# Kernel tuning notes

Measured on AMD Instinct MI355X. Metric: run time of the kernel, lower is better.

Reference implementation:

```python
import jax, jax.numpy as jnp
import numpy as np

B, S, SEG, D = 2, 128, 128, 768
RL, H, DK = 16, 8, 64
DV = D // H            # 96, dim_value = dim // heads
NRPF = D // H          # num_rel_pos_features
N = S * RL             # 2048 attention tokens
SCALE = DK ** -0.5


def setup_inputs() -> dict:
    key = jax.random.key(0)
    ks = jax.random.split(key, 12)
    g = lambda k, sh: jax.random.normal(k, sh, jnp.float32) * 0.02
    return {
        'x': jax.random.normal(ks[0], (B, S, SEG, D), jnp.float32),
        'ln_g': jnp.ones((D,), jnp.float32),
        'ln_b': jnp.zeros((D,), jnp.float32),
        'Wq': g(ks[1], (D, H * DK)),
        'Wk': g(ks[2], (D, H * DK)),
        'Wv': g(ks[3], (D, H * DV)),
        'Wr': g(ks[4], (NRPF, H * DK)),
        'r_w_bias': g(ks[5], (H, DK)),
        'r_r_bias': g(ks[6], (H, DK)),
        'Wo': g(ks[7], (H * DV, D)),
        'bo': jnp.zeros((D,), jnp.float32),
        'pos_emb': g(ks[8], (2 * N - 1, NRPF)),  # relative position features, dist -(N-1)..(N-1)
    }


def _layernorm(x, g, b, eps=1e-5):
    mu = jnp.mean(x, -1, keepdims=True)
    var = jnp.var(x, -1, keepdims=True)
    return (x - mu) * jax.lax.rsqrt(var + eps) * g + b


def _relative_shift(t):
    # t: [b, h, n, 2n-1] -> [b, h, n, n] (enformer-style shift)
    b, h, n, _ = t.shape
    t = jnp.pad(t, ((0, 0), (0, 0), (0, 0), (1, 0)))      # [b,h,n,2n]
    t = t.reshape(b, h, 2 * n, n)[:, :, 1:, :]            # [b,h,2n-1,n]
    t = t.reshape(b, h, n, 2 * n - 1)
    return t[..., :n]


def reference(x, ln_g, ln_b, Wq, Wk, Wv, Wr, r_w_bias, r_r_bias, Wo, bo, pos_emb):
    # slice representative tokens per segment and flatten: b s n d -> b (s n) d
    reps = x[:, :, :RL, :].reshape(B, N, D)
    h = _layernorm(reps, ln_g, ln_b)
    q = (h @ Wq).reshape(B, N, H, DK).transpose(0, 2, 1, 3) * SCALE  # bhnd
    k = (h @ Wk).reshape(B, N, H, DK).transpose(0, 2, 1, 3)
    v = (h @ Wv).reshape(B, N, H, DV).transpose(0, 2, 1, 3)
    content = jnp.einsum('bhid,bhjd->bhij', q + r_w_bias[None, :, None, :], k)
    rel_k = (pos_emb @ Wr).reshape(2 * N - 1, H, DK)
    rel = jnp.einsum('bhid,rhd->bhir', q + r_r_bias[None, :, None, :], rel_k)
    logits = content + _relative_shift(rel)
    attn = jax.nn.softmax(logits, axis=-1)
    out = jnp.einsum('bhij,bhjd->bhid', attn, v)
    out = out.transpose(0, 2, 1, 3).reshape(B, N, H * DV) @ Wo + bo
    reps = (reps + out).reshape(B, S, RL, D)  # residual transformer block, un-flatten
    return jnp.concatenate([reps, x[:, :, RL:, :]], axis=2)
```

## Files before the change

kernel.cpp:

```cpp
#include <hip/hip_runtime.h>

typedef short s8v __attribute__((ext_vector_type(8)));
typedef float f4 __attribute__((ext_vector_type(4)));

__device__ inline float bf2f(unsigned short u) {
  union { unsigned i; float f; } x; x.i = (unsigned)u << 16; return x.f;
}
__device__ inline unsigned short f2bf(float f) {
  union { float f; unsigned i; } x; x.f = f;
  return (unsigned short)((x.i + 0x7fffu + ((x.i >> 16) & 1u)) >> 16);
}

__device__ inline void gload16(const void* g, void* l) {
  __builtin_amdgcn_global_load_lds(
      (const __attribute__((address_space(1))) unsigned int*)g,
      (__attribute__((address_space(3))) unsigned int*)l, 16, 0, 0);
}

__global__ __launch_bounds__(256) void copy4(const float4* __restrict__ src,
                                             float4* __restrict__ dst, int n4) {
  int i = blockIdx.x * blockDim.x + threadIdx.x;
  int stride = gridDim.x * blockDim.x;
  for (; i < n4; i += stride) dst[i] = src[i];
}

__global__ __launch_bounds__(256) void ln_kernel(const float* __restrict__ x,
                                                 const float* __restrict__ g,
                                                 const float* __restrict__ bvec,
                                                 unsigned short* __restrict__ h) {
  int m = blockIdx.x;
  int b = m >> 11, n = m & 2047;
  int s = n >> 4, rl = n & 15;
  const float* row = x + ((size_t)((b * 128 + s) * 128 + rl)) * 768;
  int t = threadIdx.x;
  float v0 = row[t], v1 = row[t + 256], v2 = row[t + 512];
  float sum = v0 + v1 + v2;
  float sq = v0 * v0 + v1 * v1 + v2 * v2;
  __shared__ float rs[4], rq[4];
#pragma unroll
  for (int o = 32; o; o >>= 1) {
    sum += __shfl_down(sum, o);
    sq += __shfl_down(sq, o);
  }
  if ((t & 63) == 0) { rs[t >> 6] = sum; rq[t >> 6] = sq; }
  __syncthreads();
  sum = rs[0] + rs[1] + rs[2] + rs[3];
  sq = rq[0] + rq[1] + rq[2] + rq[3];
  float mu = sum * (1.f / 768.f);
  float var = sq * (1.f / 768.f) - mu * mu;
  float inv = rsqrtf(var + 1e-5f);
  unsigned short* hrow = h + (size_t)m * 768;
  hrow[t] = f2bf((v0 - mu) * inv * g[t] + bvec[t]);
  hrow[t + 256] = f2bf((v1 - mu) * inv * g[t + 256] + bvec[t + 256]);
  hrow[t + 512] = f2bf((v2 - mu) * inv * g[t + 512] + bvec[t + 512]);
}

__global__ __launch_bounds__(256) void transp_cvt(const float* __restrict__ Wq,
                                                  const float* __restrict__ Wk,
                                                  const float* __restrict__ Wv,
                                                  const float* __restrict__ Wo,
                                                  unsigned short* __restrict__ Bt,
                                                  unsigned short* __restrict__ Bto) {
  int z = blockIdx.z;
  const float* src; unsigned short* dst; int N;
  if (z == 0) { src = Wq; dst = Bt; N = 512; }
  else if (z == 1) { src = Wk; dst = Bt + (size_t)512 * 768; N = 512; }
  else if (z == 2) { src = Wv; dst = Bt + (size_t)1024 * 768; N = 768; }
  else { src = Wo; dst = Bto; N = 768; }
  int n0 = blockIdx.x << 6, k0 = blockIdx.y << 6;
  if (n0 >= N) return;
  __shared__ float tile[64][65];
  int t = threadIdx.x;
  int c4 = (t & 15) << 2, rr = t >> 4;
#pragma unroll
  for (int i = 0; i < 4; ++i) {
    int kr = rr + (i << 4);
    float4 v = *(const float4*)(src + (size_t)(k0 + kr) * N + n0 + c4);
    tile[c4 + 0][kr] = v.x; tile[c4 + 1][kr] = v.y;
    tile[c4 + 2][kr] = v.z; tile[c4 + 3][kr] = v.w;
  }
  __syncthreads();
  int rowN = t >> 2, kc = (t & 3) << 4;
#pragma unroll
  for (int j = 0; j < 16; ++j)
    dst[(size_t)(n0 + rowN) * 768 + k0 + kc + j] = f2bf(tile[rowN][kc + j]);
}

__global__ __launch_bounds__(256) void gemm_rel(const float* __restrict__ A,
                                                const float* __restrict__ Bw,
                                                unsigned short* __restrict__ C0,
                                                int M, int Nn, int K) {
  __shared__ float As[16][68];
  __shared__ float Bs[16][68];
  int t = threadIdx.x;
  int tx = t & 15, ty = t >> 4;
  int row0 = blockIdx.y << 6, col0 = blockIdx.x << 6;
  float acc[4][4] = {{0.f}};
  int ar = t >> 2, ac = (t & 3) << 2;
  int br = t >> 4, bc = (t & 15) << 2;
  for (int k0 = 0; k0 < K; k0 += 16) {
    float4 av = make_float4(0.f, 0.f, 0.f, 0.f);
    if (row0 + ar < M) av = *(const float4*)(A + (size_t)(row0 + ar) * K + k0 + ac);
    As[ac + 0][ar] = av.x; As[ac + 1][ar] = av.y;
    As[ac + 2][ar] = av.z; As[ac + 3][ar] = av.w;
    float4 bv = *(const float4*)(Bw + (size_t)(k0 + br) * Nn + col0 + bc);
    *(float4*)&Bs[br][bc] = bv;
    __syncthreads();
#pragma unroll
    for (int kk = 0; kk < 16; ++kk) {
      float4 a = *(const float4*)&As[kk][ty << 2];
      float4 b = *(const float4*)&Bs[kk][tx << 2];
      float arr[4] = {a.x, a.y, a.z, a.w};
      float brr[4] = {b.x, b.y, b.z, b.w};
#pragma unroll
      for (int i = 0; i < 4; ++i)
#pragma unroll
        for (int j = 0; j < 4; ++j) acc[i][j] += arr[i] * brr[j];
    }
    __syncthreads();
  }
#pragma unroll
  for (int i = 0; i < 4; ++i) {
    int r = row0 + (ty << 2) + i;
    if (r >= M) continue;
    int colb = col0 + (tx << 2);
    unsigned pk0 = f2bf(acc[i][0]) | ((unsigned)f2bf(acc[i][1]) << 16);
    unsigned pk1 = f2bf(acc[i][2]) | ((unsigned)f2bf(acc[i][3]) << 16);
    *(uint2*)(C0 + (size_t)r * Nn + colb) = make_uint2(pk0, pk1);
  }
}

template <int MODE>
__global__ __launch_bounds__(256) void gemm_mfma(
    const unsigned short* __restrict__ A, const unsigned short* __restrict__ Bt,
    unsigned short* __restrict__ qw, unsigned short* __restrict__ qr,
    unsigned short* __restrict__ kbuf, unsigned short* __restrict__ vt,
    const float* __restrict__ rwb, const float* __restrict__ rrb,
    const float* __restrict__ x, const float* __restrict__ bo,
    float* __restrict__ out) {
  __shared__ __align__(16) short As[128 * 64];
  __shared__ __align__(16) short Bs[128 * 64];
  const int t = threadIdx.x;
  const int w = t >> 6, lane = t & 63;
  const int m16 = lane & 15, quad = lane >> 4;
  const int wm = w >> 1, wn = w & 1;
  const int m0 = blockIdx.y << 7, n0 = blockIdx.x << 7;
  const int K = 768;

  f4 acc[4][4];
#pragma unroll
  for (int i = 0; i < 4; ++i)
#pragma unroll
    for (int j = 0; j < 4; ++j) acc[i][j] = (f4){0.f, 0.f, 0.f, 0.f};

  const int rA = lane >> 3;
  const int cA = lane & 7;

  for (int k0 = 0; k0 < K; k0 += 64) {
    __syncthreads();
#pragma unroll
    for (int i = 0; i < 4; ++i) {
      int seg = (w << 2) + i;
      int r = (seg << 3) + rA;
      int cg = cA ^ (r & 7);
      gload16(A + (size_t)(m0 + r) * K + k0 + (cg << 3), (short*)As + (seg << 9));
      gload16(Bt + (size_t)(n0 + r) * K + k0 + (cg << 3), (short*)Bs + (seg << 9));
    }
    __syncthreads();
#pragma unroll
    for (int kb = 0; kb < 2; ++kb) {
      int cs = ((kb << 2) + quad) ^ (m16 & 7);
      s8v af[4], bf[4];
#pragma unroll
      for (int mt = 0; mt < 4; ++mt) {
        int r = (wm << 6) + (mt << 4) + m16;
        af[mt] = *(const s8v*)(As + (r << 6) + (cs << 3));
      }
#pragma unroll
      for (int nt = 0; nt < 4; ++nt) {
        int rn = (wn << 6) + (nt << 4) + m16;
        bf[nt] = *(const s8v*)(Bs + (rn << 6) + (cs << 3));
      }
#pragma unroll
      for (int mt = 0; mt < 4; ++mt)
#pragma unroll
        for (int nt = 0; nt < 4; ++nt)
          acc[mt][nt] = __builtin_amdgcn_mfma_f32_16x16x32_bf16(af[mt], bf[nt], acc[mt][nt], 0, 0, 0);
    }
  }

#pragma unroll
  for (int nt = 0; nt < 4; ++nt) {
    int n = n0 + (wn << 6) + (nt << 4) + m16;
#pragma unroll
    for (int mt = 0; mt < 4; ++mt) {
#pragma unroll
      for (int rr = 0; rr < 4; ++rr) {
        int m = m0 + (wm << 6) + (mt << 4) + (quad << 2) + rr;
        float v = acc[mt][nt][rr];
        if (MODE == 0) {
          if (n < 512) {
            float vs = v * 0.125f;
            qw[(size_t)m * 512 + n] = f2bf(vs + rwb[n]);
            qr[(size_t)m * 512 + n] = f2bf(vs + rrb[n]);
          } else if (n < 1024) {
            kbuf[(size_t)m * 512 + (n - 512)] = f2bf(v);
          } else {
            int col = n - 1024;
            int b = m >> 11, j = m & 2047;
            vt[(((size_t)(b * 768 + col)) << 11) + j] = f2bf(v);
          }
        } else {
          int b = m >> 11, nn2 = m & 2047;
          int s = nn2 >> 4, rl = nn2 & 15;
          size_t base = ((size_t)((b * 128 + s) * 128 + rl)) * 768;
          out[base + n] = x[base + n] + v + bo[n];
        }
      }
    }
  }
}

__global__ __launch_bounds__(256) void attn_kernel(
    const unsigned short* __restrict__ qw_g, const unsigned short* __restrict__ qr_g,
    const unsigned short* __restrict__ k_g, const unsigned short* __restrict__ vt_g,
    const unsigned short* __restrict__ rk_g, unsigned short* __restrict__ ao) {
  const int qt = blockIdx.x, hh = blockIdx.y, b = blockIdx.z;
  const int i0 = qt << 5;
  const int t = threadIdx.x;
  const int lane = t & 63, w = t >> 6;
  const int m16 = lane & 15, quad = lane >> 4;
  const int mi = w & 1, njb = w >> 1;
  const int sr = t >> 3, sg = t & 7;

  __shared__ __align__(16) short qw_s[32 * 64];
  __shared__ __align__(16) short qr_s[32 * 64];
  __shared__ __align__(16) short k_s[64 * 64];
  __shared__ __align__(16) short rk_s[96 * 64];
  __shared__ __align__(16) short vt_s[96 * 64];
  __shared__ __align__(16) short pb_s[32 * 64];
  __shared__ float p_s[32][68];
  __shared__ short t_s[32][104];
  __shared__ float alpha_s[32];
  __shared__ float linv_s[32];

  for (int u = t; u < 512; u += 256) {
    int tile = u >> 8, idx = u & 255, r = idx >> 3, ch = idx & 7;
    const unsigned short* src =
        (tile ? qr_g : qw_g) + (((size_t)(b * 2048 + i0 + r)) << 9) + (hh << 6) + (ch << 3);
    int4 vdat = *(const int4*)src;
    short* dst = (tile ? qr_s : qw_s) + r * 64 + (((ch ^ (r & 7))) << 3);
    *(int4*)dst = vdat;
  }

  float m_i = -1e30f, l_i = 0.f;
  f4 o0 = {0.f, 0.f, 0.f, 0.f}, o1 = o0, o2 = o0;
  const int arow = mi * 16 + m16;
  const int asw = arow & 7;
  const int crow = mi * 16 + quad * 4;
  const int brow0 = njb * 16 + m16;
  const int bsw = brow0 & 7;

  for (int j0 = 0; j0 < 2048; j0 += 64) {
    __syncthreads();
    for (int u = t; u < 512; u += 256) {
      int r = u >> 3, ch = u & 7;
      int4 vdat = *(const int4*)(k_g + (((size_t)(b * 2048 + j0 + r)) << 9) + (hh << 6) + (ch << 3));
      *(int4*)(k_s + r * 64 + ((ch ^ (r & 7)) << 3)) = vdat;
    }
    int rbase = 2047 + j0 - i0 - 31;
    for (int u = t; u < 760; u += 256) {
      int r = u >> 3, ch = u & 7;
      int4 vdat = *(const int4*)(rk_g + (((size_t)(rbase + r)) << 9) + (hh << 6) + (ch << 3));
      *(int4*)(rk_s + r * 64 + ((ch ^ (r & 7)) << 3)) = vdat;
    }
    for (int u = t; u < 768; u += 256) {
      int r = u >> 3, ch = u & 7;
      int4 vdat =
          *(const int4*)(vt_g + (((size_t)(b * 768 + hh * 96 + r)) << 11) + j0 + (ch << 3));
      *(int4*)(vt_s + r * 64 + ((ch ^ (r & 7)) << 3)) = vdat;
    }
    __syncthreads();

    f4 c0 = {0.f, 0.f, 0.f, 0.f}, c1 = c0;
    f4 r0 = c0, r1 = c0, r2 = c0;
#pragma unroll
    for (int kb = 0; kb < 2; ++kb) {
      int co = ((kb * 4 + quad) ^ asw) << 3;
      int cb = ((kb * 4 + quad) ^ bsw) << 3;
      s8v aq = *(const s8v*)(qw_s + arow * 64 + co);
      s8v ar = *(const s8v*)(qr_s + arow * 64 + co);
      s8v bk0 = *(const s8v*)(k_s + brow0 * 64 + cb);
      s8v bk1 = *(const s8v*)(k_s + (brow0 + 32) * 64 + cb);
      c0 = __builtin_amdgcn_mfma_f32_16x16x32_bf16(aq, bk0, c0, 0, 0, 0);
      c1 = __builtin_amdgcn_mfma_f32_16x16x32_bf16(aq, bk1, c1, 0, 0, 0);
      s8v br0 = *(const s8v*)(rk_s + brow0 * 64 + cb);
      s8v br1 = *(const s8v*)(rk_s + (brow0 + 32) * 64 + cb);
      s8v br2 = *(const s8v*)(rk_s + (brow0 + 64) * 64 + cb);
      r0 = __builtin_amdgcn_mfma_f32_16x16x32_bf16(ar, br0, r0, 0, 0, 0);
      r1 = __builtin_amdgcn_mfma_f32_16x16x32_bf16(ar, br1, r1, 0, 0, 0);
      r2 = __builtin_amdgcn_mfma_f32_16x16x32_bf16(ar, br2, r2, 0, 0, 0);
    }
#pragma unroll
    for (int rr = 0; rr < 4; ++rr) {
      p_s[crow + rr][njb * 16 + m16] = c0[rr];
      p_s[crow + rr][(njb + 2) * 16 + m16] = c1[rr];
      t_s[crow + rr][njb * 16 + m16] = (short)f2bf(r0[rr]);
      t_s[crow + rr][(njb + 2) * 16 + m16] = (short)f2bf(r1[rr]);
      t_s[crow + rr][(njb + 4) * 16 + m16] = (short)f2bf(r2[rr]);
    }
    __syncthreads();

    float sv[8];
    float mx = -1e30f;
#pragma unroll
    for (int j2 = 0; j2 < 8; ++j2) {
      int c = sg + (j2 << 3);
      float s = p_s[sr][c] + bf2f((unsigned short)t_s[sr][c - sr + 31]);
      sv[j2] = s;
      mx = fmaxf(mx, s);
    }
    mx = fmaxf(mx, __shfl_xor(mx, 1));
    mx = fmaxf(mx, __shfl_xor(mx, 2));
    mx = fmaxf(mx, __shfl_xor(mx, 4));
    float m_new = fmaxf(m_i, mx);
    float al = __expf(m_i - m_new);
    float sm = 0.f;
#pragma unroll
    for (int j2 = 0; j2 < 8; ++j2) {
      float p = __expf(sv[j2] - m_new);
      sm += p;
      pb_s[sr * 64 + ((j2 ^ (sr & 7)) << 3) + sg] = (short)f2bf(p);
    }
    sm += __shfl_xor(sm, 1);
    sm += __shfl_xor(sm, 2);
    sm += __shfl_xor(sm, 4);
    l_i = l_i * al + sm;
    m_i = m_new;
    if (sg == 0) alpha_s[sr] = al;
    __syncthreads();

#pragma unroll
    for (int rr = 0; rr < 4; ++rr) {
      float a = alpha_s[crow + rr];
      o0[rr] *= a; o1[rr] *= a; o2[rr] *= a;
    }
#pragma unroll
    for (int kb = 0; kb < 2; ++kb) {
      int co = ((kb * 4 + quad) ^ asw) << 3;
      int cb = ((kb * 4 + quad) ^ bsw) << 3;
      s8v ap = *(const s8v*)(pb_s + arow * 64 + co);
      s8v b0v = *(const s8v*)(vt_s + brow0 * 64 + cb);
      s8v b1v = *(const s8v*)(vt_s + (brow0 + 32) * 64 + cb);
      s8v b2v = *(const s8v*)(vt_s + (brow0 + 64) * 64 + cb);
      o0 = __builtin_amdgcn_mfma_f32_16x16x32_bf16(ap, b0v, o0, 0, 0, 0);
      o1 = __builtin_amdgcn_mfma_f32_16x16x32_bf16(ap, b1v, o1, 0, 0, 0);
      o2 = __builtin_amdgcn_mfma_f32_16x16x32_bf16(ap, b2v, o2, 0, 0, 0);
    }
  }

  if (sg == 0) linv_s[sr] = 1.f / l_i;
  __syncthreads();
#pragma unroll
  for (int rr = 0; rr < 4; ++rr) {
    int row = crow + rr;
    float inv = linv_s[row];
    size_t gbase = ((size_t)(b * 2048 + i0 + row)) * 768 + hh * 96;
    ao[gbase + njb * 16 + m16] = f2bf(o0[rr] * inv);
    ao[gbase + (njb + 2) * 16 + m16] = f2bf(o1[rr] * inv);
    ao[gbase + (njb + 4) * 16 + m16] = f2bf(o2[rr] * inv);
  }
}

extern "C" void kernel_launch(void* const* d_in, const int* in_sizes, int n_in,
                              void* d_out, int out_size, void* d_ws, size_t ws_size,
                              hipStream_t stream) {
  (void)in_sizes; (void)n_in; (void)out_size; (void)ws_size;
  const float* x = (const float*)d_in[0];
  const float* ln_g = (const float*)d_in[1];
  const float* ln_b = (const float*)d_in[2];
  const float* Wq = (const float*)d_in[3];
  const float* Wk = (const float*)d_in[4];
  const float* Wv = (const float*)d_in[5];
  const float* Wr = (const float*)d_in[6];
  const float* rwb = (const float*)d_in[7];
  const float* rrb = (const float*)d_in[8];
  const float* Wo = (const float*)d_in[9];
  const float* bo = (const float*)d_in[10];
  const float* pe = (const float*)d_in[11];
  float* out = (float*)d_out;

  char* p = (char*)d_ws;
  unsigned short* hbf = (unsigned short*)p; p += (size_t)4096 * 768 * 2;
  unsigned short* qw = (unsigned short*)p;  p += (size_t)4096 * 512 * 2;
  unsigned short* qr = (unsigned short*)p;  p += (size_t)4096 * 512 * 2;
  unsigned short* kb = (unsigned short*)p;  p += (size_t)4096 * 512 * 2;
  unsigned short* vt = (unsigned short*)p;  p += (size_t)4096 * 768 * 2;
  unsigned short* rk = (unsigned short*)p;  p += (size_t)4095 * 512 * 2;
  unsigned short* ao = (unsigned short*)p;  p += (size_t)4096 * 768 * 2;
  unsigned short* Bt = (unsigned short*)p;  p += (size_t)1792 * 768 * 2;
  unsigned short* Bto = (unsigned short*)p;

  transp_cvt<<<dim3(12, 12, 4), dim3(256), 0, stream>>>(Wq, Wk, Wv, Wo, Bt, Bto);
  copy4<<<dim3(2048), dim3(256), 0, stream>>>((const float4*)x, (float4*)out, 6291456);
  ln_kernel<<<dim3(4096), dim3(256), 0, stream>>>(x, ln_g, ln_b, hbf);
  gemm_rel<<<dim3(8, 64), dim3(256), 0, stream>>>(pe, Wr, rk, 4095, 512, 96);
  gemm_mfma<0><<<dim3(14, 32), dim3(256), 0, stream>>>(hbf, Bt, qw, qr, kb, vt, rwb, rrb,
                                                       nullptr, nullptr, nullptr);
  attn_kernel<<<dim3(64, 8, 2), dim3(256), 0, stream>>>(qw, qr, kb, vt, rk, ao);
  gemm_mfma<1><<<dim3(6, 32), dim3(256), 0, stream>>>(ao, Bto, nullptr, nullptr, nullptr,
                                                      nullptr, nullptr, nullptr, x, bo, out);
}
```

Baseline: 504.7 us.

## Load K, rel-K and V MFMA operands directly from global memory, dropping LDS staging

Removes the LDS staging buffers for K, relative-key and transposed-V tiles. Each wave now reads its MFMA B operands straight from global memory, which removes two barriers per iteration and frees shared memory for higher occupancy. It also adds s_setprio around the MFMA groups and clamps the last rel-key row to avoid reading out of bounds. The cost is redundant global/L2 traffic, since each operand is read by multiple waves and blocks, and global-load latency is now exposed with no prefetching.

```diff
diff --git a/kernel.cpp b/kernel.cpp
--- a/kernel.cpp
+++ b/kernel.cpp
@@ -235,9 +235,6 @@
 
   __shared__ __align__(16) short qw_s[32 * 64];
   __shared__ __align__(16) short qr_s[32 * 64];
-  __shared__ __align__(16) short k_s[64 * 64];
-  __shared__ __align__(16) short rk_s[96 * 64];
-  __shared__ __align__(16) short vt_s[96 * 64];
   __shared__ __align__(16) short pb_s[32 * 64];
   __shared__ float p_s[32][68];
   __shared__ short t_s[32][104];
@@ -252,6 +249,7 @@
     short* dst = (tile ? qr_s : qw_s) + r * 64 + (((ch ^ (r & 7))) << 3);
     *(int4*)dst = vdat;
   }
+  __syncthreads();
 
   float m_i = -1e30f, l_i = 0.f;
   f4 o0 = {0.f, 0.f, 0.f, 0.f}, o1 = o0, o2 = o0;
@@ -259,47 +257,39 @@
   const int asw = arow & 7;
   const int crow = mi * 16 + quad * 4;
   const int brow0 = njb * 16 + m16;
-  const int bsw = brow0 & 7;
+
+  const unsigned short* kbase = k_g + (((size_t)(b * 2048 + brow0)) << 9) + (hh << 6);
+  const unsigned short* vbase = vt_g + (((size_t)(b * 768 + hh * 96 + brow0)) << 11);
 
   for (int j0 = 0; j0 < 2048; j0 += 64) {
-    __syncthreads();
-    for (int u = t; u < 512; u += 256) {
-      int r = u >> 3, ch = u & 7;
-      int4 vdat = *(const int4*)(k_g + (((size_t)(b * 2048 + j0 + r)) << 9) + (hh << 6) + (ch << 3));
-      *(int4*)(k_s + r * 64 + ((ch ^ (r & 7)) << 3)) = vdat;
-    }
-    int rbase = 2047 + j0 - i0 - 31;
-    for (int u = t; u < 760; u += 256) {
-      int r = u >> 3, ch = u & 7;
-      int4 vdat = *(const int4*)(rk_g + (((size_t)(rbase + r)) << 9) + (hh << 6) + (ch << 3));
-      *(int4*)(rk_s + r * 64 + ((ch ^ (r & 7)) << 3)) = vdat;
-    }
-    for (int u = t; u < 768; u += 256) {
-      int r = u >> 3, ch = u & 7;
-      int4 vdat =
-          *(const int4*)(vt_g + (((size_t)(b * 768 + hh * 96 + r)) << 11) + j0 + (ch << 3));
-      *(int4*)(vt_s + r * 64 + ((ch ^ (r & 7)) << 3)) = vdat;
-    }
-    __syncthreads();
+    const int rbase = 2047 + j0 - i0 - 31;
+    int r2row = rbase + brow0 + 64;
+    if (r2row > 4094) r2row = 4094;
+    const unsigned short* kk = kbase + ((size_t)j0 << 9);
+    const unsigned short* rb0 = rk_g + (((size_t)(rbase + brow0)) << 9) + (hh << 6);
+    const unsigned short* rb1 = rk_g + (((size_t)(rbase + brow0 + 32)) << 9) + (hh << 6);
+    const unsigned short* rb2 = rk_g + (((size_t)r2row) << 9) + (hh << 6);
 
     f4 c0 = {0.f, 0.f, 0.f, 0.f}, c1 = c0;
     f4 r0 = c0, r1 = c0, r2 = c0;
 #pragma unroll
     for (int kb = 0; kb < 2; ++kb) {
-      int co = ((kb * 4 + quad) ^ asw) << 3;
-      int cb = ((kb * 4 + quad) ^ bsw) << 3;
+      const int cidx = (kb << 2) + quad;
+      const int co = (cidx ^ asw) << 3;
       s8v aq = *(const s8v*)(qw_s + arow * 64 + co);
       s8v ar = *(const s8v*)(qr_s + arow * 64 + co);
-      s8v bk0 = *(const s8v*)(k_s + brow0 * 64 + cb);
-      s8v bk1 = *(const s8v*)(k_s + (brow0 + 32) * 64 + cb);
+      s8v bk0 = *(const s8v*)(kk + (cidx << 3));
+      s8v bk1 = *(const s8v*)(kk + ((size_t)32 << 9) + (cidx << 3));
+      s8v br0 = *(const s8v*)(rb0 + (cidx << 3));
+      s8v br1 = *(const s8v*)(rb1 + (cidx << 3));
+      s8v br2 = *(const s8v*)(rb2 + (cidx << 3));
+      __builtin_amdgcn_s_setprio(1);
       c0 = __builtin_amdgcn_mfma_f32_16x16x32_bf16(aq, bk0, c0, 0, 0, 0);
       c1 = __builtin_amdgcn_mfma_f32_16x16x32_bf16(aq, bk1, c1, 0, 0, 0);
-      s8v br0 = *(const s8v*)(rk_s + brow0 * 64 + cb);
-      s8v br1 = *(const s8v*)(rk_s + (brow0 + 32) * 64 + cb);
-      s8v br2 = *(const s8v*)(rk_s + (brow0 + 64) * 64 + cb);
       r0 = __builtin_amdgcn_mfma_f32_16x16x32_bf16(ar, br0, r0, 0, 0, 0);
       r1 = __builtin_amdgcn_mfma_f32_16x16x32_bf16(ar, br1, r1, 0, 0, 0);
       r2 = __builtin_amdgcn_mfma_f32_16x16x32_bf16(ar, br2, r2, 0, 0, 0);
+      __builtin_amdgcn_s_setprio(0);
     }
 #pragma unroll
     for (int rr = 0; rr < 4; ++rr) {
@@ -345,17 +335,20 @@
       float a = alpha_s[crow + rr];
       o0[rr] *= a; o1[rr] *= a; o2[rr] *= a;
     }
+    const unsigned short* vb = vbase + j0;
 #pragma unroll
     for (int kb = 0; kb < 2; ++kb) {
-      int co = ((kb * 4 + quad) ^ asw) << 3;
-      int cb = ((kb * 4 + quad) ^ bsw) << 3;
+      const int cidx = (kb << 2) + quad;
+      const int co = (cidx ^ asw) << 3;
       s8v ap = *(const s8v*)(pb_s + arow * 64 + co);
-      s8v b0v = *(const s8v*)(vt_s + brow0 * 64 + cb);
-      s8v b1v = *(const s8v*)(vt_s + (brow0 + 32) * 64 + cb);
-      s8v b2v = *(const s8v*)(vt_s + (brow0 + 64) * 64 + cb);
+      s8v b0v = *(const s8v*)(vb + (cidx << 3));
+      s8v b1v = *(const s8v*)(vb + ((size_t)32 << 11) + (cidx << 3));
+      s8v b2v = *(const s8v*)(vb + ((size_t)64 << 11) + (cidx << 3));
+      __builtin_amdgcn_s_setprio(1);
       o0 = __builtin_amdgcn_mfma_f32_16x16x32_bf16(ap, b0v, o0, 0, 0, 0);
       o1 = __builtin_amdgcn_mfma_f32_16x16x32_bf16(ap, b1v, o1, 0, 0, 0);
       o2 = __builtin_amdgcn_mfma_f32_16x16x32_bf16(ap, b2v, o2, 0, 0, 0);
+      __builtin_amdgcn_s_setprio(0);
     }
   }
 
```

New measurement: 514.9 us. 1.02x slower.
